# Kernel tuning notes

Measured on AMD Instinct MI355X. Metric: run time of the kernel, lower is better.

## Reference

```python
import jax, jax.numpy as jnp
import numpy as np

N = 20000      # nodes
E = 320000     # edges (avg degree 16)
IN = 512       # input feature dim
HID = 64       # hidden_dim
NH = 8         # n_heads
NC = 20        # n_classes
NG = 64        # graphs in batch
EPS = 1e-5     # batchnorm eps


def setup_inputs() -> dict:
    key = jax.random.key(0)
    ks = jax.random.split(key, 32)
    rn = lambda k, shape, s=0.05: (jax.random.normal(k, shape, jnp.float32) * s)
    inp = {
        "x": rn(ks[0], (N, IN), 1.0),
        "src": jax.random.randint(ks[1], (E,), 0, N),
        "dst": jax.random.randint(ks[2], (E,), 0, N),
        "graph_ids": jnp.sort(jax.random.randint(ks[3], (N,), 0, NG)),
        "n_graphs": NG,
        # encoder
        "W_enc": rn(ks[4], (IN, HID)), "b_enc": jnp.zeros((HID,), jnp.float32),
        # GAT layer 0
        "fc_W0": rn(ks[5], (HID, NH * HID)),
        "attn_l0": rn(ks[6], (NH, HID)), "attn_r0": rn(ks[7], (NH, HID)),
        "res_W0": rn(ks[8], (HID, NH * HID)),
        "bias0": jnp.zeros((NH * HID,), jnp.float32),
        "dp_W0": rn(ks[9], (NH * HID, HID)), "dp_b0": jnp.zeros((HID,), jnp.float32),
        # GAT layer 1
        "fc_W1": rn(ks[10], (HID, NH * HID)),
        "attn_l1": rn(ks[11], (NH, HID)), "attn_r1": rn(ks[12], (NH, HID)),
        "res_W1": rn(ks[13], (HID, NH * HID)),
        "bias1": jnp.zeros((NH * HID,), jnp.float32),
        "dp_W1": rn(ks[14], (NH * HID, HID)), "dp_b1": jnp.zeros((HID,), jnp.float32),
        # batchnorm affine
        "gamma": jnp.ones((2 * HID,), jnp.float32), "beta": jnp.zeros((2 * HID,), jnp.float32),
        # global attention pooling gate
        "gate_W": rn(ks[15], (2 * HID, 1)), "gate_b": jnp.zeros((1,), jnp.float32),
        # classifier
        "cls_W": rn(ks[16], (2 * HID, NC)), "cls_b": jnp.zeros((NC,), jnp.float32),
    }
    return inp


def gat_conv(h, fc_W, attn_l, attn_r, res_W, bias, src, dst, n_nodes):
    # DGL GATConv: fc -> per-head scalar scores -> edge softmax over incoming
    # edges -> weighted sum -> residual + bias -> leaky_relu activation.
    nh, d = attn_l.shape
    feat = (h @ fc_W).reshape(n_nodes, nh, d)              # [N,H,D]
    el = jnp.sum(feat * attn_l[None], axis=-1)             # [N,H]
    er = jnp.sum(feat * attn_r[None], axis=-1)             # [N,H]
    e = jax.nn.leaky_relu(el[src] + er[dst], 0.2)          # [E,H]
    m = jax.ops.segment_max(e, dst, num_segments=n_nodes)  # segment softmax
    ex = jnp.exp(e - m[dst])
    denom = jax.ops.segment_sum(ex, dst, num_segments=n_nodes)
    a = ex / denom[dst]                                    # [E,H]
    msg = feat[src] * a[:, :, None]                        # [E,H,D]  (dominant)
    rst = jax.ops.segment_sum(msg, dst, num_segments=n_nodes)  # [N,H,D]
    rst = rst + (h @ res_W).reshape(n_nodes, nh, d) + bias.reshape(nh, d)
    return jax.nn.leaky_relu(rst, 0.01)  # F.leaky_relu default slope


def reference(x, W_enc, b_enc,
              fc_W0, attn_l0, attn_r0, res_W0, bias0, dp_W0, dp_b0,
              fc_W1, attn_l1, attn_r1, res_W1, bias1, dp_W1, dp_b1,
              gamma, beta, gate_W, gate_b, cls_W, cls_b,
              src, dst, graph_ids, n_graphs):
    n_nodes = x.shape[0]
    he = x @ W_enc + b_enc                                  # encoder [N,HID]
    h = he
    h = gat_conv(h, fc_W0, attn_l0, attn_r0, res_W0, bias0, src, dst, n_nodes)
    h = h.reshape(n_nodes, -1) @ dp_W0 + dp_b0              # down_proj 0
    h = gat_conv(h, fc_W1, attn_l1, attn_r1, res_W1, bias1, src, dst, n_nodes)
    h = h.reshape(n_nodes, -1) @ dp_W1 + dp_b1              # down_proj 1
    hg = jnp.concatenate([h, he], axis=1)                   # [N,2*HID]
    # BatchNorm1d (training-mode batch stats, biased variance)
    mu = jnp.mean(hg, axis=0)
    var = jnp.var(hg, axis=0)
    hg = (hg - mu) * jax.lax.rsqrt(var + EPS) * gamma + beta
    # GlobalAttentionPooling: per-graph softmax over node gates
    gate = hg @ gate_W + gate_b                             # [N,1]
    gm = jax.ops.segment_max(gate, graph_ids, num_segments=n_graphs)
    ge = jnp.exp(gate - gm[graph_ids])
    gden = jax.ops.segment_sum(ge, graph_ids, num_segments=n_graphs)
    alpha = ge / gden[graph_ids]                            # [N,1]
    readout = jax.ops.segment_sum(alpha * hg, graph_ids, num_segments=n_graphs)
    return readout @ cls_W + cls_b                          # [NG,NC]
```

## Files before the change

### kernel.cpp

```cpp
#include <hip/hip_runtime.h>
#include <hip/hip_bf16.h>

#define MROWS   20000
#define N_EDGES 320000
#define DIN     512
#define HID     64
#define NH      8
#define ND      512
#define NCLS    20
#define NG      64
#define BN_EPS  1e-5f
#define PCH     16
#define BNB     256
#define TPB     128
#define AGG_NBLK  125
#define AGG_CHUNK 160

typedef __hip_bfloat16 bf16;
typedef __attribute__((ext_vector_type(8))) short s16x8;
typedef __attribute__((ext_vector_type(4))) short s16x4;
typedef __attribute__((ext_vector_type(4))) float f32x4;

enum { TF32 = 0, TBF16 = 1, TMODE = 2 };

__device__ __forceinline__ int is_bf16_mode(const void* gamma) {
    return *(const unsigned*)gamma != 0x3F800000u;
}

__device__ __forceinline__ float ld_f32(const void* p, size_t i) { return ((const float*)p)[i]; }
__device__ __forceinline__ float ld_b16(const void* p, size_t i) { return __bfloat162float(((const bf16*)p)[i]); }

template<int T>
__device__ __forceinline__ float ldT(const void* p, size_t i, int bf) {
    if constexpr (T == TF32) return ld_f32(p, i);
    else if constexpr (T == TBF16) return ld_b16(p, i);
    else return bf ? ld_b16(p, i) : ld_f32(p, i);
}
template<int T>
__device__ __forceinline__ void stT(void* p, size_t i, int bf, float v) {
    if constexpr (T == TF32) ((float*)p)[i] = v;
    else if constexpr (T == TBF16) ((bf16*)p)[i] = __float2bfloat16(v);
    else { if (bf) ((bf16*)p)[i] = __float2bfloat16(v); else ((float*)p)[i] = v; }
}

__device__ __forceinline__ float bfbits2f(short s) {
    return __uint_as_float(((unsigned)(unsigned short)s) << 16);
}
__device__ __forceinline__ short f2bfbits(float v) {
    bf16 b = __float2bfloat16(v);
    return *reinterpret_cast<short*>(&b);
}

struct TP { const void* src[7]; bf16* dst[7]; int K[7]; };
__global__ void prep_kernel(TP tp, const void* __restrict__ gamma, int* __restrict__ zero0) {
    int b = blockIdx.x;
    int z = b * 256 + threadIdx.x;
    if (z < 2 * MROWS) zero0[z] = 0;
    const int bf = is_bf16_mode(gamma);
    int id = b / TPB;
    int i = (b - id * TPB) * 256 + threadIdx.x;
    int K = tp.K[id];
    int N = (DIN * HID) / K;
    int n = i / K, k = i - n * K;
    tp.dst[id][i] = __float2bfloat16(ldT<TMODE>(tp.src[id], (size_t)k * N + n, bf));
}

__global__ void hist_kernel(const int* __restrict__ keys, int* __restrict__ counts, int n) {
    int i = blockIdx.x * 256 + threadIdx.x;
    if (i < n) atomicAdd(&counts[keys[i]], 1);
}

__global__ __launch_bounds__(1024)
void scan_all_kernel(const int* __restrict__ counts, int* __restrict__ offs,
                     const int* __restrict__ gids, int* __restrict__ goffs) {
    if (threadIdx.x <= NG) {
        int g = threadIdx.x;
        int lo = 0, hi = MROWS;
        while (lo < hi) {
            int mid = (lo + hi) >> 1;
            if (gids[mid] < g) lo = mid + 1; else hi = mid;
        }
        goffs[g] = lo;
    }
    __shared__ int wsum[16];
    __shared__ int carry_s;
    int carry = 0;
    int lane = threadIdx.x & 63, wid = threadIdx.x >> 6;
    const int NCHUNK = (MROWS + 1023) / 1024;
    for (int ch = 0; ch < NCHUNK; ++ch) {
        int i = ch * 1024 + threadIdx.x;
        int v = (i < MROWS) ? counts[i] : 0;
        int s = v;
        #pragma unroll
        for (int o = 1; o < 64; o <<= 1) { int t = __shfl_up(s, o, 64); if (lane >= o) s += t; }
        if (lane == 63) wsum[wid] = s;
        __syncthreads();
        if (wid == 0 && lane < 16) {
            int t = wsum[lane];
            #pragma unroll
            for (int o = 1; o < 16; o <<= 1) { int u = __shfl_up(t, o, 64); if (lane >= o) t += u; }
            wsum[lane] = t;
        }
        __syncthreads();
        int wc = (wid > 0) ? wsum[wid - 1] : 0;
        int incl = s + wc + carry;
        if (i < MROWS) offs[i] = incl - v;
        if (threadIdx.x == 1023) carry_s = incl;
        __syncthreads();
        carry = carry_s;
    }
    if (threadIdx.x == 0) offs[MROWS] = carry;
}

__global__ void scatter_kernel(const int* __restrict__ src, const int* __restrict__ dst,
                               const int* __restrict__ offs, int* __restrict__ cursor,
                               int* __restrict__ src_sorted) {
    int e = blockIdx.x * 256 + threadIdx.x;
    if (e < N_EDGES) {
        int d = dst[e];
        int pos = offs[d] + atomicAdd(&cursor[d], 1);
        src_sorted[pos] = src[e];
    }
}

template<int K, int NB, int NTOT, bool XF32>
__global__ __launch_bounds__(256)
void gemm_mfma(const void* __restrict__ Araw, const bf16* __restrict__ BT,
               const void* __restrict__ bias, bf16* __restrict__ C,
               const void* __restrict__ gamma) {
    const int bf = is_bf16_mode(gamma);
    const int wid  = threadIdx.x >> 6;
    const int lane = threadIdx.x & 63;
    const int quad = lane >> 4;
    const int l16  = lane & 15;
    const int rb = blockIdx.x * 128 + wid * 32;
    const int cb = blockIdx.y * NB;
    constexpr int CT = NB / 16;
    constexpr int KC = K / 32;

    f32x4 acc[2][CT] = {};
    int r0 = rb + l16;       if (r0 >= MROWS) r0 = MROWS - 1;
    int r1 = rb + 16 + l16;  if (r1 >= MROWS) r1 = MROWS - 1;

    auto lda = [&](int row, int koff) -> s16x8 {
        if (XF32 && !bf) {
            const float* fp = (const float*)Araw + (size_t)row * K + koff;
            float4 u = *(const float4*)fp;
            float4 v = *(const float4*)(fp + 4);
            s16x8 r;
            r[0] = f2bfbits(u.x); r[1] = f2bfbits(u.y); r[2] = f2bfbits(u.z); r[3] = f2bfbits(u.w);
            r[4] = f2bfbits(v.x); r[5] = f2bfbits(v.y); r[6] = f2bfbits(v.z); r[7] = f2bfbits(v.w);
            return r;
        }
        return *(const s16x8*)((const bf16*)Araw + (size_t)row * K + koff);
    };
    const bf16* btp = BT + (size_t)(cb + l16) * K + quad * 8;

    for (int kc = 0; kc < KC; ++kc) {
        s16x8 af0 = lda(r0, quad * 8 + kc * 32);
        s16x8 af1 = lda(r1, quad * 8 + kc * 32);
        s16x8 bfr[CT];
        #pragma unroll
        for (int ct = 0; ct < CT; ++ct)
            bfr[ct] = *(const s16x8*)(btp + (size_t)ct * 16 * K + kc * 32);
        #pragma unroll
        for (int ct = 0; ct < CT; ++ct) {
            acc[0][ct] = __builtin_amdgcn_mfma_f32_16x16x32_bf16(bfr[ct], af0, acc[0][ct], 0, 0, 0);
            acc[1][ct] = __builtin_amdgcn_mfma_f32_16x16x32_bf16(bfr[ct], af1, acc[1][ct], 0, 0, 0);
        }
    }
    #pragma unroll
    for (int ct = 0; ct < CT; ++ct) {
        int c0 = cb + ct * 16 + quad * 4;
        float b0 = bias ? ldT<TMODE>(bias, c0 + 0, bf) : 0.f;
        float b1 = bias ? ldT<TMODE>(bias, c0 + 1, bf) : 0.f;
        float b2 = bias ? ldT<TMODE>(bias, c0 + 2, bf) : 0.f;
        float b3 = bias ? ldT<TMODE>(bias, c0 + 3, bf) : 0.f;
        #pragma unroll
        for (int rt = 0; rt < 2; ++rt) {
            int row = rb + rt * 16 + l16;
            if (row < MROWS) {
                s16x4 o;
                o[0] = f2bfbits(acc[rt][ct][0] + b0);
                o[1] = f2bfbits(acc[rt][ct][1] + b1);
                o[2] = f2bfbits(acc[rt][ct][2] + b2);
                o[3] = f2bfbits(acc[rt][ct][3] + b3);
                *(s16x4*)(C + (size_t)row * NTOT + c0) = o;
            }
        }
    }
}

__global__ __launch_bounds__(256)
void gemm_fcres(const bf16* __restrict__ A, const bf16* __restrict__ BT_fc,
                const bf16* __restrict__ BT_res, const void* __restrict__ bias,
                const void* __restrict__ attn_l, const void* __restrict__ attn_r,
                bf16* __restrict__ feat, bf16* __restrict__ rst,
                float* __restrict__ el, float* __restrict__ er,
                const void* __restrict__ gamma) {
    const int bf = is_bf16_mode(gamma);
    const bool isres = blockIdx.y >= 4;
    const int yy = blockIdx.y & 3;
    const bf16* BT = isres ? BT_res : BT_fc;
    bf16* C = isres ? rst : feat;
    const int wid  = threadIdx.x >> 6;
    const int lane = threadIdx.x & 63;
    const int quad = lane >> 4;
    const int l16  = lane & 15;
    const int rb = blockIdx.x * 128 + wid * 32;
    const int cb = yy * 128;
    constexpr int CT = 8;
    constexpr int K  = HID;
    constexpr int KC = K / 32;

    f32x4 acc[2][CT] = {};
    int r0 = rb + l16;       if (r0 >= MROWS) r0 = MROWS - 1;
    int r1 = rb + 16 + l16;  if (r1 >= MROWS) r1 = MROWS - 1;
    const bf16* a0p = A + (size_t)r0 * K + quad * 8;
    const bf16* a1p = A + (size_t)r1 * K + quad * 8;
    const bf16* btp = BT + (size_t)(cb + l16) * K + quad * 8;

    #pragma unroll
    for (int kc = 0; kc < KC; ++kc) {
        s16x8 af0 = *(const s16x8*)(a0p + kc * 32);
        s16x8 af1 = *(const s16x8*)(a1p + kc * 32);
        s16x8 bfr[CT];
        #pragma unroll
        for (int ct = 0; ct < CT; ++ct)
            bfr[ct] = *(const s16x8*)(btp + (size_t)ct * 16 * K + kc * 32);
        #pragma unroll
        for (int ct = 0; ct < CT; ++ct) {
            acc[0][ct] = __builtin_amdgcn_mfma_f32_16x16x32_bf16(bfr[ct], af0, acc[0][ct], 0, 0, 0);
            acc[1][ct] = __builtin_amdgcn_mfma_f32_16x16x32_bf16(bfr[ct], af1, acc[1][ct], 0, 0, 0);
        }
    }
    #pragma unroll
    for (int ct = 0; ct < CT; ++ct) {
        int c0 = cb + ct * 16 + quad * 4;
        float b0 = isres ? ldT<TMODE>(bias, c0 + 0, bf) : 0.f;
        float b1 = isres ? ldT<TMODE>(bias, c0 + 1, bf) : 0.f;
        float b2 = isres ? ldT<TMODE>(bias, c0 + 2, bf) : 0.f;
        float b3 = isres ? ldT<TMODE>(bias, c0 + 3, bf) : 0.f;
        #pragma unroll
        for (int rt = 0; rt < 2; ++rt) {
            int row = rb + rt * 16 + l16;
            if (row < MROWS) {
                s16x4 o;
                o[0] = f2bfbits(acc[rt][ct][0] + b0);
                o[1] = f2bfbits(acc[rt][ct][1] + b1);
                o[2] = f2bfbits(acc[rt][ct][2] + b2);
                o[3] = f2bfbits(acc[rt][ct][3] + b3);
                *(s16x4*)(C + (size_t)row * ND + c0) = o;
            }
        }
    }
    if (!isres) {
        #pragma unroll
        for (int rt = 0; rt < 2; ++rt) {
            float e0 = 0.f, f0 = 0.f, e1 = 0.f, f1 = 0.f;
            #pragma unroll
            for (int ct = 0; ct < 4; ++ct) {
                int c0 = cb + ct * 16 + quad * 4;
                int c1 = c0 + 64;
                #pragma unroll
                for (int rg = 0; rg < 4; ++rg) {
                    e0 += acc[rt][ct][rg]     * ldT<TMODE>(attn_l, c0 + rg, bf);
                    f0 += acc[rt][ct][rg]     * ldT<TMODE>(attn_r, c0 + rg, bf);
                    e1 += acc[rt][ct + 4][rg] * ldT<TMODE>(attn_l, c1 + rg, bf);
                    f1 += acc[rt][ct + 4][rg] * ldT<TMODE>(attn_r, c1 + rg, bf);
                }
            }
            e0 += __shfl_xor(e0, 16, 64); e0 += __shfl_xor(e0, 32, 64);
            f0 += __shfl_xor(f0, 16, 64); f0 += __shfl_xor(f0, 32, 64);
            e1 += __shfl_xor(e1, 16, 64); e1 += __shfl_xor(e1, 32, 64);
            f1 += __shfl_xor(f1, 16, 64); f1 += __shfl_xor(f1, 32, 64);
            int row = rb + rt * 16 + l16;
            if (row < MROWS) {
                if (quad == 0)      el[row * 8 + 2 * yy]     = e0;
                else if (quad == 1) el[row * 8 + 2 * yy + 1] = e1;
                else if (quad == 2) er[row * 8 + 2 * yy]     = f0;
                else                er[row * 8 + 2 * yy + 1] = f1;
            }
        }
    }
}

__global__ __launch_bounds__(256)
void agg_kernel(const bf16* __restrict__ feat, const float* __restrict__ el,
                const float* __restrict__ er, const int* __restrict__ offs,
                const int* __restrict__ srcs, bf16* __restrict__ rst) {
    const int b = blockIdx.x;
    const int hx = b & 7;
    const int chunk = b >> 3;
    const int g = threadIdx.x >> 3;
    const int l8 = threadIdx.x & 7;
    const int base = hx * 64 + l8 * 8;

    for (int n = chunk * AGG_CHUNK + g; n < (chunk + 1) * AGG_CHUNK; n += 32) {
        int e0 = offs[n], e1 = offs[n + 1];
        float er_h = er[n * 8 + hx];
        float acc[8] = {0.f, 0.f, 0.f, 0.f, 0.f, 0.f, 0.f, 0.f};
        float den = 0.f;
        for (int eb = e0; eb < e1; eb += 4) {
            int last = e1 - 1;
            int i1 = eb + 1 > last ? last : eb + 1;
            int i2 = eb + 2 > last ? last : eb + 2;
            int i3 = eb + 3 > last ? last : eb + 3;
            int s0 = srcs[eb], s1 = srcs[i1], s2 = srcs[i2], s3 = srcs[i3];
            float l0 = el[s0 * 8 + hx], l1 = el[s1 * 8 + hx];
            float l2 = el[s2 * 8 + hx], l3 = el[s3 * 8 + hx];
            s16x8 f0 = *(const s16x8*)(feat + (size_t)s0 * ND + base);
            s16x8 f1 = *(const s16x8*)(feat + (size_t)s1 * ND + base);
            s16x8 f2 = *(const s16x8*)(feat + (size_t)s2 * ND + base);
            s16x8 f3 = *(const s16x8*)(feat + (size_t)s3 * ND + base);
            float sc0 = l0 + er_h; sc0 = sc0 > 0.f ? sc0 : 0.2f * sc0;
            float sc1 = l1 + er_h; sc1 = sc1 > 0.f ? sc1 : 0.2f * sc1;
            float sc2 = l2 + er_h; sc2 = sc2 > 0.f ? sc2 : 0.2f * sc2;
            float sc3 = l3 + er_h; sc3 = sc3 > 0.f ? sc3 : 0.2f * sc3;
            float w0 = __expf(fminf(sc0, 30.f));
            float w1 = __expf(fminf(sc1, 30.f));
            float w2 = __expf(fminf(sc2, 30.f));
            float w3 = __expf(fminf(sc3, 30.f));
            int rem = e1 - eb;
            if (rem < 4) {
                if (rem < 2) w1 = 0.f;
                if (rem < 3) w2 = 0.f;
                w3 = 0.f;
            }
            den += w0 + w1 + w2 + w3;
            #pragma unroll
            for (int j = 0; j < 8; ++j)
                acc[j] += bfbits2f(f0[j]) * w0 + bfbits2f(f1[j]) * w1
                        + bfbits2f(f2[j]) * w2 + bfbits2f(f3[j]) * w3;
        }
        float inv = (den > 0.f) ? 1.f / den : 0.f;
        s16x8* rp = (s16x8*)(rst + (size_t)n * ND + base);
        s16x8 rr = *rp;
        s16x8 ro;
        #pragma unroll
        for (int j = 0; j < 8; ++j) {
            float r = bfbits2f(rr[j]) + acc[j] * inv;
            r = r > 0.f ? r : 0.01f * r;
            ro[j] = f2bfbits(r);
        }
        *rp = ro;
    }
}

__global__ void bn_part_kernel(const bf16* __restrict__ h2, const bf16* __restrict__ he,
                               float* __restrict__ psum, float* __restrict__ psq) {
    int t = threadIdx.x;
    int b = blockIdx.x;
    int beg = (int)((long)MROWS * b / BNB);
    int end = (int)((long)MROWS * (b + 1) / BNB);
    const bf16* srcb = (t < 64) ? h2 : he;
    int col = t & 63;
    float s = 0.f, s2 = 0.f;
    for (int r = beg; r < end; ++r) {
        float v = __bfloat162float(srcb[(size_t)r * 64 + col]);
        s += v;
        s2 += v * v;
    }
    psum[b * 128 + t] = s;
    psq[b * 128 + t] = s2;
}

__global__ void bn_reduce_kernel(const float* __restrict__ psum, const float* __restrict__ psq,
                                 const void* __restrict__ gamma, const void* __restrict__ beta,
                                 float* __restrict__ scale, float* __restrict__ shift) {
    const int bf = is_bf16_mode(gamma);
    int t = threadIdx.x;
    float s = 0.f, s2 = 0.f;
    for (int b = 0; b < BNB; ++b) { s += psum[b * 128 + t]; s2 += psq[b * 128 + t]; }
    float mu = s * (1.f / MROWS);
    float var = s2 * (1.f / MROWS) - mu * mu;
    float inv = rsqrtf(fmaxf(var, 0.f) + BN_EPS);
    float a = ldT<TMODE>(gamma, t, bf) * inv;
    scale[t] = a;
    shift[t] = ldT<TMODE>(beta, t, bf) - mu * a;
}

__global__ __launch_bounds__(128)
void poolgate_kernel(const bf16* __restrict__ h2, const bf16* __restrict__ he,
                     const float* __restrict__ scale, const float* __restrict__ shift,
                     const void* __restrict__ gate_W, const void* __restrict__ gate_b,
                     const int* __restrict__ goffs,
                     float* __restrict__ pacc, float* __restrict__ pden,
                     const void* __restrict__ gamma) {
    const int bf = is_bf16_mode(gamma);
    int g = blockIdx.x;
    int c = blockIdx.y;
    int t = threadIdx.x;
    int r0 = goffs[g], r1 = goffs[g + 1];
    int len = r1 - r0;
    int beg = r0 + (int)((long)len * c / PCH);
    int end = r0 + (int)((long)len * (c + 1) / PCH);
    const bf16* srcb = (t < 64) ? h2 : he;
    int col = t & 63;
    float sc = scale[t], sh = shift[t];
    float gw = ldT<TMODE>(gate_W, t, bf);
    float gb = ldT<TMODE>(gate_b, 0, bf);
    __shared__ float ws[2];
    float acc = 0.f, den = 0.f;
    for (int r = beg; r < end; ++r) {
        float v = __bfloat162float(srcb[(size_t)r * 64 + col]) * sc + sh;
        float p = v * gw;
        #pragma unroll
        for (int o = 32; o > 0; o >>= 1) p += __shfl_xor(p, o, 64);
        if ((t & 63) == 0) ws[t >> 6] = p;
        __syncthreads();
        float wg = __expf(fminf(fmaxf(ws[0] + ws[1] + gb, -60.f), 30.f));
        den += wg;
        acc += wg * v;
        __syncthreads();
    }
    pacc[((size_t)g * PCH + c) * 128 + t] = acc;
    if (t == 0) pden[g * PCH + c] = den;
}

__global__ __launch_bounds__(128)
void poolcls_kernel(const float* __restrict__ pacc, const float* __restrict__ pden,
                    const void* __restrict__ W, const void* __restrict__ b,
                    void* __restrict__ out, const void* __restrict__ gamma) {
    const int bf = is_bf16_mode(gamma);
    int g = blockIdx.x;
    int t = threadIdx.x;
    float acc = 0.f, den = 0.f;
    #pragma unroll
    for (int c = 0; c < PCH; ++c) {
        acc += pacc[((size_t)g * PCH + c) * 128 + t];
        den += pden[g * PCH + c];
    }
    __shared__ float rs[128];
    rs[t] = (den > 0.f) ? acc / den : 0.f;
    __syncthreads();
    if (t < NCLS) {
        float o = ldT<TMODE>(b, t, bf);
        #pragma unroll 8
        for (int k = 0; k < 128; ++k)
            o += rs[k] * ldT<TMODE>(W, (size_t)k * NCLS + t, bf);
        stT<TMODE>(out, g * NCLS + t, bf, o);
    }
}

extern "C" void kernel_launch(void* const* d_in, const int* in_sizes, int n_in,
                              void* d_out, int out_size, void* d_ws, size_t ws_size,
                              hipStream_t stream) {
    const void* x       = d_in[0];
    const int*  src     = (const int*)d_in[1];
    const int*  dst     = (const int*)d_in[2];
    const int*  gids    = (const int*)d_in[3];
    const void* W_enc   = d_in[5];
    const void* b_enc   = d_in[6];
    const void* fc_W0   = d_in[7];
    const void* attn_l0 = d_in[8];
    const void* attn_r0 = d_in[9];
    const void* res_W0  = d_in[10];
    const void* bias0   = d_in[11];
    const void* dp_W0   = d_in[12];
    const void* dp_b0   = d_in[13];
    const void* fc_W1   = d_in[14];
    const void* attn_l1 = d_in[15];
    const void* attn_r1 = d_in[16];
    const void* res_W1  = d_in[17];
    const void* bias1   = d_in[18];
    const void* dp_W1   = d_in[19];
    const void* dp_b1   = d_in[20];
    const void* gamma   = d_in[21];
    const void* beta    = d_in[22];
    const void* gate_W  = d_in[23];
    const void* gate_b  = d_in[24];
    const void* cls_W   = d_in[25];
    const void* cls_b   = d_in[26];

    char* wsc = (char*)d_ws;
    size_t off = 0;
    auto alloc = [&](size_t bytes) -> void* {
        void* p = wsc + off;
        off = (off + bytes + 255) & ~(size_t)255;
        return p;
    };
    bf16*  he        = (bf16*) alloc((size_t)MROWS * HID * 2);
    bf16*  h         = (bf16*) alloc((size_t)MROWS * HID * 2);
    bf16*  h2        = (bf16*) alloc((size_t)MROWS * HID * 2);
    bf16*  feat      = (bf16*) alloc((size_t)MROWS * ND * 2);
    bf16*  rst       = (bf16*) alloc((size_t)MROWS * ND * 2);
    bf16*  bt_enc    = (bf16*) alloc((size_t)DIN * HID * 2);
    bf16*  bt_fc0    = (bf16*) alloc((size_t)HID * ND * 2);
    bf16*  bt_res0   = (bf16*) alloc((size_t)HID * ND * 2);
    bf16*  bt_dp0    = (bf16*) alloc((size_t)ND * HID * 2);
    bf16*  bt_fc1    = (bf16*) alloc((size_t)HID * ND * 2);
    bf16*  bt_res1   = (bf16*) alloc((size_t)HID * ND * 2);
    bf16*  bt_dp1    = (bf16*) alloc((size_t)ND * HID * 2);
    float* el        = (float*)alloc((size_t)MROWS * 8 * 4);
    float* er        = (float*)alloc((size_t)MROWS * 8 * 4);
    int*   src_sorted= (int*)  alloc((size_t)N_EDGES * 4);
    int*   offs      = (int*)  alloc((size_t)(MROWS + 1) * 4);
    int*   goffs     = (int*)  alloc((size_t)(NG + 1) * 4);
    float* psum      = (float*)alloc((size_t)BNB * 128 * 4);
    float* psq       = (float*)alloc((size_t)BNB * 128 * 4);
    float* pacc      = (float*)alloc((size_t)NG * PCH * 128 * 4);
    float* pden      = (float*)alloc((size_t)NG * PCH * 4);
    float* bnscale   = (float*)alloc(128 * 4);
    float* bnshift   = (float*)alloc(128 * 4);
    char*  zbase     = (char*) alloc((size_t)MROWS * 4 * 2);
    int* counts  = (int*)zbase;
    int* cursor  = counts + MROWS;

    TP tp;
    tp.src[0] = W_enc;  tp.K[0] = DIN;
    tp.src[1] = fc_W0;  tp.K[1] = HID;
    tp.src[2] = res_W0; tp.K[2] = HID;
    tp.src[3] = dp_W0;  tp.K[3] = ND;
    tp.src[4] = fc_W1;  tp.K[4] = HID;
    tp.src[5] = res_W1; tp.K[5] = HID;
    tp.src[6] = dp_W1;  tp.K[6] = ND;
    tp.dst[0] = bt_enc; tp.dst[1] = bt_fc0; tp.dst[2] = bt_res0; tp.dst[3] = bt_dp0;
    tp.dst[4] = bt_fc1; tp.dst[5] = bt_res1; tp.dst[6] = bt_dp1;
    prep_kernel<<<7 * TPB, 256, 0, stream>>>(tp, gamma, (int*)zbase);

    hist_kernel<<<(N_EDGES + 255) / 256, 256, 0, stream>>>(dst, counts, N_EDGES);
    scan_all_kernel<<<1, 1024, 0, stream>>>(counts, offs, gids, goffs);
    scatter_kernel<<<(N_EDGES + 255) / 256, 256, 0, stream>>>(src, dst, offs, cursor, src_sorted);

    const int GX = (MROWS + 127) / 128;

    gemm_mfma<DIN, 64, 64, true><<<dim3(GX, 1), 256, 0, stream>>>(x, bt_enc, b_enc, he, gamma);

    gemm_fcres<<<dim3(GX, 8), 256, 0, stream>>>(he, bt_fc0, bt_res0, bias0, attn_l0, attn_r0,
                                                feat, rst, el, er, gamma);
    agg_kernel<<<AGG_NBLK * 8, 256, 0, stream>>>(feat, el, er, offs, src_sorted, rst);
    gemm_mfma<ND, 64, 64, false><<<dim3(GX, 1), 256, 0, stream>>>(rst, bt_dp0, dp_b0, h, gamma);

    gemm_fcres<<<dim3(GX, 8), 256, 0, stream>>>(h, bt_fc1, bt_res1, bias1, attn_l1, attn_r1,
                                                feat, rst, el, er, gamma);
    agg_kernel<<<AGG_NBLK * 8, 256, 0, stream>>>(feat, el, er, offs, src_sorted, rst);
    gemm_mfma<ND, 64, 64, false><<<dim3(GX, 1), 256, 0, stream>>>(rst, bt_dp1, dp_b1, h2, gamma);

    bn_part_kernel<<<BNB, 128, 0, stream>>>(h2, he, psum, psq);
    bn_reduce_kernel<<<1, 128, 0, stream>>>(psum, psq, gamma, beta, bnscale, bnshift);
    poolgate_kernel<<<dim3(NG, PCH), 128, 0, stream>>>(h2, he, bnscale, bnshift, gate_W, gate_b,
                                                       goffs, pacc, pden, gamma);
    poolcls_kernel<<<NG, 128, 0, stream>>>(pacc, pden, cls_W, cls_b, d_out, gamma);
}
```

Measured before the change: 468.3 us.

## Compute residual projection inside aggregation kernel instead of the fc/res GEMM

The residual projection (h @ res_W + bias) is moved out of the MFMA GEMM kernel and recomputed per node inside the edge aggregation kernel with scalar FMAs. The fc GEMM grid is halved, and the agg kernel no longer reads back a 20000x512 bf16 residual buffer that the GEMM had written. In exchange each agg thread does 512 scalar multiply-adds per node, with weight rows reloaded from global/L2 instead of using tensor cores, which may make the agg kernel compute-bound.

```diff
diff --git a/kernel.cpp b/kernel.cpp
--- a/kernel.cpp
+++ b/kernel.cpp
@@ -193,16 +193,12 @@
 
 __global__ __launch_bounds__(256)
 void gemm_fcres(const bf16* __restrict__ A, const bf16* __restrict__ BT_fc,
-                const bf16* __restrict__ BT_res, const void* __restrict__ bias,
                 const void* __restrict__ attn_l, const void* __restrict__ attn_r,
-                bf16* __restrict__ feat, bf16* __restrict__ rst,
+                bf16* __restrict__ feat,
                 float* __restrict__ el, float* __restrict__ er,
                 const void* __restrict__ gamma) {
     const int bf = is_bf16_mode(gamma);
-    const bool isres = blockIdx.y >= 4;
-    const int yy = blockIdx.y & 3;
-    const bf16* BT = isres ? BT_res : BT_fc;
-    bf16* C = isres ? rst : feat;
+    const int yy = blockIdx.y;
     const int wid  = threadIdx.x >> 6;
     const int lane = threadIdx.x & 63;
     const int quad = lane >> 4;
@@ -218,7 +214,7 @@
     int r1 = rb + 16 + l16;  if (r1 >= MROWS) r1 = MROWS - 1;
     const bf16* a0p = A + (size_t)r0 * K + quad * 8;
     const bf16* a1p = A + (size_t)r1 * K + quad * 8;
-    const bf16* btp = BT + (size_t)(cb + l16) * K + quad * 8;
+    const bf16* btp = BT_fc + (size_t)(cb + l16) * K + quad * 8;
 
     #pragma unroll
     for (int kc = 0; kc < KC; ++kc) {
@@ -237,50 +233,44 @@
     #pragma unroll
     for (int ct = 0; ct < CT; ++ct) {
         int c0 = cb + ct * 16 + quad * 4;
-        float b0 = isres ? ldT<TMODE>(bias, c0 + 0, bf) : 0.f;
-        float b1 = isres ? ldT<TMODE>(bias, c0 + 1, bf) : 0.f;
-        float b2 = isres ? ldT<TMODE>(bias, c0 + 2, bf) : 0.f;
-        float b3 = isres ? ldT<TMODE>(bias, c0 + 3, bf) : 0.f;
         #pragma unroll
         for (int rt = 0; rt < 2; ++rt) {
             int row = rb + rt * 16 + l16;
             if (row < MROWS) {
                 s16x4 o;
-                o[0] = f2bfbits(acc[rt][ct][0] + b0);
-                o[1] = f2bfbits(acc[rt][ct][1] + b1);
-                o[2] = f2bfbits(acc[rt][ct][2] + b2);
-                o[3] = f2bfbits(acc[rt][ct][3] + b3);
-                *(s16x4*)(C + (size_t)row * ND + c0) = o;
+                o[0] = f2bfbits(acc[rt][ct][0]);
+                o[1] = f2bfbits(acc[rt][ct][1]);
+                o[2] = f2bfbits(acc[rt][ct][2]);
+                o[3] = f2bfbits(acc[rt][ct][3]);
+                *(s16x4*)(feat + (size_t)row * ND + c0) = o;
             }
         }
     }
-    if (!isres) {
-        #pragma unroll
-        for (int rt = 0; rt < 2; ++rt) {
-            float e0 = 0.f, f0 = 0.f, e1 = 0.f, f1 = 0.f;
+    #pragma unroll
+    for (int rt = 0; rt < 2; ++rt) {
+        float e0 = 0.f, f0 = 0.f, e1 = 0.f, f1 = 0.f;
+        #pragma unroll
+        for (int ct = 0; ct < 4; ++ct) {
+            int c0 = cb + ct * 16 + quad * 4;
+            int c1 = c0 + 64;
             #pragma unroll
-            for (int ct = 0; ct < 4; ++ct) {
-                int c0 = cb + ct * 16 + quad * 4;
-                int c1 = c0 + 64;
-                #pragma unroll
-                for (int rg = 0; rg < 4; ++rg) {
-                    e0 += acc[rt][ct][rg]     * ldT<TMODE>(attn_l, c0 + rg, bf);
-                    f0 += acc[rt][ct][rg]     * ldT<TMODE>(attn_r, c0 + rg, bf);
-                    e1 += acc[rt][ct + 4][rg] * ldT<TMODE>(attn_l, c1 + rg, bf);
-                    f1 += acc[rt][ct + 4][rg] * ldT<TMODE>(attn_r, c1 + rg, bf);
-                }
+            for (int rg = 0; rg < 4; ++rg) {
+                e0 += acc[rt][ct][rg]     * ldT<TMODE>(attn_l, c0 + rg, bf);
+                f0 += acc[rt][ct][rg]     * ldT<TMODE>(attn_r, c0 + rg, bf);
+                e1 += acc[rt][ct + 4][rg] * ldT<TMODE>(attn_l, c1 + rg, bf);
+                f1 += acc[rt][ct + 4][rg] * ldT<TMODE>(attn_r, c1 + rg, bf);
             }
-            e0 += __shfl_xor(e0, 16, 64); e0 += __shfl_xor(e0, 32, 64);
-            f0 += __shfl_xor(f0, 16, 64); f0 += __shfl_xor(f0, 32, 64);
-            e1 += __shfl_xor(e1, 16, 64); e1 += __shfl_xor(e1, 32, 64);
-            f1 += __shfl_xor(f1, 16, 64); f1 += __shfl_xor(f1, 32, 64);
-            int row = rb + rt * 16 + l16;
-            if (row < MROWS) {
-                if (quad == 0)      el[row * 8 + 2 * yy]     = e0;
-                else if (quad == 1) el[row * 8 + 2 * yy + 1] = e1;
-                else if (quad == 2) er[row * 8 + 2 * yy]     = f0;
-                else                er[row * 8 + 2 * yy + 1] = f1;
-            }
+        }
+        e0 += __shfl_xor(e0, 16, 64); e0 += __shfl_xor(e0, 32, 64);
+        f0 += __shfl_xor(f0, 16, 64); f0 += __shfl_xor(f0, 32, 64);
+        e1 += __shfl_xor(e1, 16, 64); e1 += __shfl_xor(e1, 32, 64);
+        f1 += __shfl_xor(f1, 16, 64); f1 += __shfl_xor(f1, 32, 64);
+        int row = rb + rt * 16 + l16;
+        if (row < MROWS) {
+            if (quad == 0)      el[row * 8 + 2 * yy]     = e0;
+            else if (quad == 1) el[row * 8 + 2 * yy + 1] = e1;
+            else if (quad == 2) er[row * 8 + 2 * yy]     = f0;
+            else                er[row * 8 + 2 * yy + 1] = f1;
         }
     }
 }
@@ -288,7 +278,11 @@
 __global__ __launch_bounds__(256)
 void agg_kernel(const bf16* __restrict__ feat, const float* __restrict__ el,
                 const float* __restrict__ er, const int* __restrict__ offs,
-                const int* __restrict__ srcs, bf16* __restrict__ rst) {
+                const int* __restrict__ srcs,
+                const bf16* __restrict__ A, const bf16* __restrict__ bt_res,
+                const void* __restrict__ bias,
+                bf16* __restrict__ rst, const void* __restrict__ gamma) {
+    const int bf = is_bf16_mode(gamma);
     const int b = blockIdx.x;
     const int hx = b & 7;
     const int chunk = b >> 3;
@@ -333,17 +327,29 @@
                 acc[j] += bfbits2f(f0[j]) * w0 + bfbits2f(f1[j]) * w1
                         + bfbits2f(f2[j]) * w2 + bfbits2f(f3[j]) * w3;
         }
+        float rr[8];
+        #pragma unroll
+        for (int j = 0; j < 8; ++j) rr[j] = ldT<TMODE>(bias, base + j, bf);
+        #pragma unroll
+        for (int kc = 0; kc < 8; ++kc) {
+            s16x8 hv = *(const s16x8*)(A + (size_t)n * HID + kc * 8);
+            #pragma unroll
+            for (int j = 0; j < 8; ++j) {
+                s16x8 wv = *(const s16x8*)(bt_res + (size_t)(base + j) * HID + kc * 8);
+                #pragma unroll
+                for (int t = 0; t < 8; ++t)
+                    rr[j] += bfbits2f(hv[t]) * bfbits2f(wv[t]);
+            }
+        }
         float inv = (den > 0.f) ? 1.f / den : 0.f;
-        s16x8* rp = (s16x8*)(rst + (size_t)n * ND + base);
-        s16x8 rr = *rp;
         s16x8 ro;
         #pragma unroll
         for (int j = 0; j < 8; ++j) {
-            float r = bfbits2f(rr[j]) + acc[j] * inv;
+            float r = rr[j] + acc[j] * inv;
             r = r > 0.f ? r : 0.01f * r;
             ro[j] = f2bfbits(r);
         }
-        *rp = ro;
+        *(s16x8*)(rst + (size_t)n * ND + base) = ro;
     }
 }
 
@@ -527,14 +533,16 @@
 
     gemm_mfma<DIN, 64, 64, true><<<dim3(GX, 1), 256, 0, stream>>>(x, bt_enc, b_enc, he, gamma);
 
-    gemm_fcres<<<dim3(GX, 8), 256, 0, stream>>>(he, bt_fc0, bt_res0, bias0, attn_l0, attn_r0,
-                                                feat, rst, el, er, gamma);
-    agg_kernel<<<AGG_NBLK * 8, 256, 0, stream>>>(feat, el, er, offs, src_sorted, rst);
+    gemm_fcres<<<dim3(GX, 4), 256, 0, stream>>>(he, bt_fc0, attn_l0, attn_r0,
+                                                feat, el, er, gamma);
+    agg_kernel<<<AGG_NBLK * 8, 256, 0, stream>>>(feat, el, er, offs, src_sorted,
+                                                 he, bt_res0, bias0, rst, gamma);
     gemm_mfma<ND, 64, 64, false><<<dim3(GX, 1), 256, 0, stream>>>(rst, bt_dp0, dp_b0, h, gamma);
 
-    gemm_fcres<<<dim3(GX, 8), 256, 0, stream>>>(h, bt_fc1, bt_res1, bias1, attn_l1, attn_r1,
-                                                feat, rst, el, er, gamma);
-    agg_kernel<<<AGG_NBLK * 8, 256, 0, stream>>>(feat, el, er, offs, src_sorted, rst);
+    gemm_fcres<<<dim3(GX, 4), 256, 0, stream>>>(h, bt_fc1, attn_l1, attn_r1,
+                                                feat, el, er, gamma);
+    agg_kernel<<<AGG_NBLK * 8, 256, 0, stream>>>(feat, el, er, offs, src_sorted,
+                                                 h, bt_res1, bias1, rst, gamma);
     gemm_mfma<ND, 64, 64, false><<<dim3(GX, 1), 256, 0, stream>>>(rst, bt_dp1, dp_b1, h2, gamma);
 
     bn_part_kernel<<<BNB, 128, 0, stream>>>(h2, he, psum, psq);
```

After: 1.058 ms. 126% more time.
